# Optimization experiments

Hardware: AMD Instinct MI355X
Metric: run time of the kernel (lower is better)

Reference implementation:

```python
import jax, jax.numpy as jnp
import numpy as np

N_NODES = 100000
N_EDGES = 1600000
EMB = 128
N_LAYERS = 3
BN_EPS = 1e-5


def setup_inputs() -> dict:
    key = jax.random.key(0)
    k1, k2, k3 = jax.random.split(key, 3)
    feats = jax.random.normal(k1, (N_NODES, EMB), dtype=jnp.float32)
    edge_index = jax.random.randint(k2, (2, N_EDGES), 0, N_NODES, dtype=jnp.int64)
    # Glorot-ish scaled weights per layer
    W = jax.random.normal(k3, (N_LAYERS, EMB, EMB), dtype=jnp.float32) * (1.0 / np.sqrt(EMB))
    b = jnp.zeros((N_LAYERS, EMB), dtype=jnp.float32)
    gamma = jnp.ones((N_LAYERS, EMB), dtype=jnp.float32)
    beta = jnp.zeros((N_LAYERS, EMB), dtype=jnp.float32)
    return {"feats": feats, "edge_index": edge_index, "W": W, "b": b, "gamma": gamma, "beta": beta}


def _gcn_layer(h, row, col, W_l, b_l):
    # GCNConv (add_self_loops=False, normalize=True): x = h @ W, symmetric-norm scatter-add, + bias
    x = h @ W_l  # [N, D]
    ones = jnp.ones((row.shape[0],), dtype=h.dtype)
    deg = jax.ops.segment_sum(ones, col, num_segments=N_NODES)  # in-degree of targets
    dinv = jnp.where(deg > 0, jax.lax.rsqrt(jnp.maximum(deg, 1.0)), 0.0)
    norm = dinv[row] * dinv[col]  # [E]
    msg = x[row] * norm[:, None]  # gather + scale, [E, D]
    out = jax.ops.segment_sum(msg, col, num_segments=N_NODES)  # scatter-add
    return out + b_l


def _batch_norm(h, gamma_l, beta_l):
    mu = jnp.mean(h, axis=0)
    var = jnp.mean(jnp.square(h - mu), axis=0)  # biased var (torch BN training math)
    return (h - mu) * jax.lax.rsqrt(var + BN_EPS) * gamma_l + beta_l


def reference(feats, edge_index, W, b, gamma, beta):
    row, col = edge_index[0], edge_index[1]  # source, target
    h = feats
    for l in range(N_LAYERS):
        h = _gcn_layer(h, row, col, W[l], b[l])
        h = _batch_norm(h, gamma[l], beta[l])
        # dropout treated as identity (eval mode); residual=False; JK='last'
    return h
```

## Files before the change

### kernel.cpp

```cpp
#include <hip/hip_runtime.h>
#include <cstdint>
#include <cstddef>

#define BN_EPS 1e-5f
#define NCHUNK 256
#define WT_PITCH 136

typedef short bf16x8 __attribute__((ext_vector_type(8)));
typedef float f32x4 __attribute__((ext_vector_type(4)));


__device__ __forceinline__ int edge_at(const void* e, long long i, int m64) {
  return m64 ? (int)((const long long*)e)[i] : ((const int*)e)[i];
}

__device__ __forceinline__ unsigned short f2bf(float f) {
  unsigned int u = __float_as_uint(f);
  unsigned int r = (u + 0x7FFFu + ((u >> 16) & 1u)) >> 16;
  return (unsigned short)r;
}

__device__ __forceinline__ unsigned int pack2bf(float lo, float hi) {
  return (unsigned int)f2bf(lo) | ((unsigned int)f2bf(hi) << 16);
}

__global__ void detect_kernel(const int* __restrict__ e, int* __restrict__ mode) {
  int nz = 0;
  for (int i = 1; i < 512; i += 2) nz |= e[i];
  mode[0] = (nz == 0) ? 1 : 0;
}


__global__ __launch_bounds__(256) void count_kernel(const void* __restrict__ edges,
                                                    const int* __restrict__ mode,
                                                    int* __restrict__ blockcounts,
                                                    int E, int nb, int chunk) {
  __shared__ int h[1024];
  int m = mode[0];
  for (int i = threadIdx.x; i < nb; i += 256) h[i] = 0;
  __syncthreads();
  long long lo = (long long)blockIdx.x * chunk;
  long long hi = lo + chunk;
  if (hi > E) hi = E;
  for (long long i = lo + threadIdx.x; i < hi; i += 256) {
    int c = edge_at(edges, (long long)E + i, m);
    atomicAdd(&h[c >> 8], 1);
  }
  __syncthreads();
  for (int j = threadIdx.x; j < nb; j += 256)
    blockcounts[(size_t)j * NCHUNK + blockIdx.x] = h[j];
}

__global__ __launch_bounds__(256) void scan1_kernel(const int* __restrict__ src,
                                                    int* __restrict__ tprefix,
                                                    int* __restrict__ bsum, int n) {
  __shared__ int s[256];
  int t = threadIdx.x;
  int gid = blockIdx.x * 256 + t;
  int base = gid * 4;
  int sum = 0;
#pragma unroll
  for (int j = 0; j < 4; j++) {
    int i = base + j;
    if (i < n) sum += src[i];
  }
  s[t] = sum;
  __syncthreads();
  for (int off = 1; off < 256; off <<= 1) {
    int v = (t >= off) ? s[t - off] : 0;
    __syncthreads();
    s[t] += v;
    __syncthreads();
  }
  tprefix[gid] = s[t] - sum;
  if (t == 255) bsum[blockIdx.x] = s[255];
}

__global__ __launch_bounds__(256) void scan2_kernel(int* __restrict__ bsum, int nbk,
                                                    int* __restrict__ out, int n) {
  __shared__ int s[256];
  int t = threadIdx.x;
  int v = (t < nbk) ? bsum[t] : 0;
  s[t] = v;
  __syncthreads();
  for (int off = 1; off < 256; off <<= 1) {
    int u = (t >= off) ? s[t - off] : 0;
    __syncthreads();
    s[t] += u;
    __syncthreads();
  }
  if (t < nbk) bsum[t] = s[t] - v;
  if (t == 255) out[n] = s[255];
}

__global__ __launch_bounds__(256) void scan3_kernel(const int* __restrict__ src,
                                                    const int* __restrict__ tprefix,
                                                    const int* __restrict__ bsum,
                                                    int* __restrict__ out, int n) {
  int gid = blockIdx.x * 256 + threadIdx.x;
  int run = bsum[blockIdx.x] + tprefix[gid];
  int base = gid * 4;
#pragma unroll
  for (int j = 0; j < 4; j++) {
    int i = base + j;
    if (i < n) {
      int c = src[i];
      out[i] = run;
      run += c;
    }
  }
}

__global__ __launch_bounds__(256) void scatter_kernel(const void* __restrict__ edges,
                                                      const int* __restrict__ mode,
                                                      const int* __restrict__ moff,
                                                      int* __restrict__ pairs,
                                                      int E, int nb, int chunk) {
  __shared__ int cur[1024];
  int m = mode[0];
  for (int j = threadIdx.x; j < nb; j += 256)
    cur[j] = moff[(size_t)j * NCHUNK + blockIdx.x];
  __syncthreads();
  long long lo = (long long)blockIdx.x * chunk;
  long long hi = lo + chunk;
  if (hi > E) hi = E;
  for (long long i = lo + threadIdx.x; i < hi; i += 256) {
    int r = edge_at(edges, i, m);
    int c = edge_at(edges, (long long)E + i, m);
    int pos = atomicAdd(&cur[c >> 8], 1);
    pairs[pos] = (r << 8) | (c & 255);
  }
}

__global__ __launch_bounds__(256) void passB12_kernel(const int* __restrict__ pairs,
                                                      const int* __restrict__ moff,
                                                      float* __restrict__ dinv,
                                                      int* __restrict__ offsets,
                                                      int* __restrict__ csr_row, int n) {
  __shared__ int h[256];
  __shared__ int s[256];
  int t = threadIdx.x;
  int b = blockIdx.x;
  h[t] = 0;
  __syncthreads();
  int lo = moff[(size_t)b * NCHUNK];
  int hi = moff[(size_t)(b + 1) * NCHUNK];
  for (int e = lo + t; e < hi; e += 256)
    atomicAdd(&h[pairs[e] & 255], 1);
  __syncthreads();
  int d = h[t];
  s[t] = d;
  __syncthreads();
  for (int off = 1; off < 256; off <<= 1) {
    int v = (t >= off) ? s[t - off] : 0;
    __syncthreads();
    s[t] += v;
    __syncthreads();
  }
  int start = lo + s[t] - d;
  int node = b * 256 + t;
  if (node < n) {
    offsets[node] = start;
    dinv[node] = d > 0 ? rsqrtf((float)d) : 0.f;
    if (node == n - 1) offsets[n] = hi;
  }
  s[t] = start;
  __syncthreads();
  for (int e = lo + t; e < hi; e += 256) {
    int p = pairs[e];
    int pos = atomicAdd(&s[p & 255], 1);
    csr_row[pos] = p >> 8;
  }
}

__global__ __launch_bounds__(256) void prepWR_kernel(const float* __restrict__ W,
                                                     const float* __restrict__ colstats,
                                                     const float* __restrict__ gamma,
                                                     const float* __restrict__ beta,
                                                     float invN, int use_affine,
                                                     unsigned short* __restrict__ Wt,
                                                     float* __restrict__ rbias) {
  __shared__ float sc[128], sh[128];
  int t = threadIdx.x;
  if (t < 128) {
    float scv = 1.f, shv = 0.f;
    if (use_affine) {
      float mu = colstats[t] * invN;
      float var = colstats[128 + t] * invN - mu * mu;
      var = fmaxf(var, 0.f);
      scv = gamma[t] * rsqrtf(var + BN_EPS);
      shv = beta[t] - mu * scv;
    }
    sc[t] = scv;
    sh[t] = shv;
  }
  __syncthreads();
  int idx = blockIdx.x * 256 + t;
  int nc = idx >> 7, k = idx & 127;
  Wt[(size_t)nc * 128 + k] = f2bf(W[(size_t)k * 128 + nc] * sc[k]);
  if (blockIdx.x == 0 && t < 128) {
    float s = 0.f;
    if (use_affine) {
      for (int kk = 0; kk < 128; kk++) s += sh[kk] * W[(size_t)kk * 128 + t];
    }
    rbias[t] = s;
  }
}

template <int A_IS_FP32>
__global__ __launch_bounds__(256) void gemm_mfma_kernel(
    const void* __restrict__ Ain, const unsigned short* __restrict__ Wt,
    const float* __restrict__ rbias, const float* __restrict__ dinv,
    unsigned short* __restrict__ xb, int n) {
  __shared__ unsigned short wt[128 * WT_PITCH];
  int t = threadIdx.x;
  {
    int row = t >> 1, half = t & 1;
    const uint4* src = (const uint4*)(Wt + (size_t)row * 128 + half * 64);
    uint4* dst = (uint4*)(wt + row * WT_PITCH + half * 64);
#pragma unroll
    for (int j = 0; j < 8; j++) dst[j] = src[j];
  }
  __syncthreads();

  int l = t & 63;
  int w = t >> 6;
  int kg = l >> 4;

  for (int sub = 0; sub < 2; sub++) {
    int row0 = blockIdx.x * 128 + sub * 64 + w * 16;
    if (row0 >= n) break;
    int m = row0 + (l & 15);
    int mc = m < n ? m : n - 1;

    bf16x8 b[4];
#pragma unroll
    for (int kk = 0; kk < 4; kk++) {
      if (A_IS_FP32) {
        const float* ap = (const float*)Ain + (size_t)mc * 128 + kk * 32 + kg * 8;
        float4 f0 = *(const float4*)ap;
        float4 f1 = *(const float4*)(ap + 4);
        bf16x8 bb;
        bb[0] = (short)f2bf(f0.x); bb[1] = (short)f2bf(f0.y);
        bb[2] = (short)f2bf(f0.z); bb[3] = (short)f2bf(f0.w);
        bb[4] = (short)f2bf(f1.x); bb[5] = (short)f2bf(f1.y);
        bb[6] = (short)f2bf(f1.z); bb[7] = (short)f2bf(f1.w);
        b[kk] = bb;
      } else {
        b[kk] = *(const bf16x8*)((const unsigned short*)Ain + (size_t)mc * 128 + kk * 32 + kg * 8);
      }
    }

    f32x4 acc[8];
#pragma unroll
    for (int nt = 0; nt < 8; nt++) {
      f32x4 zv = {0.f, 0.f, 0.f, 0.f};
      acc[nt] = zv;
    }

#pragma unroll
    for (int kk = 0; kk < 4; kk++) {
#pragma unroll
      for (int nt = 0; nt < 8; nt++) {
        bf16x8 a = *(const bf16x8*)(wt + (size_t)(nt * 16 + (l & 15)) * WT_PITCH + kk * 32 + kg * 8);
        acc[nt] = __builtin_amdgcn_mfma_f32_16x16x32_bf16(a, b[kk], acc[nt], 0, 0, 0);
      }
    }

    float dv = dinv[mc];
    int colbase = kg * 4;
#pragma unroll
    for (int nt = 0; nt < 8; nt++) {
      int c0 = nt * 16 + colbase;
      float4 rb = *(const float4*)&rbias[c0];
      unsigned int w0 = pack2bf((acc[nt][0] + rb.x) * dv, (acc[nt][1] + rb.y) * dv);
      unsigned int w1 = pack2bf((acc[nt][2] + rb.z) * dv, (acc[nt][3] + rb.w) * dv);
      if (m < n)
        *(uint2*)(xb + (size_t)m * 128 + c0) = make_uint2(w0, w1);
    }
  }
}

template <int F32OUT>
__global__ __launch_bounds__(256) void agg_kernel(
    const uint4* __restrict__ x4, const int* __restrict__ csr_row,
    const int* __restrict__ offsets, const float* __restrict__ dinv,
    void* __restrict__ z, int n) {
  int node = blockIdx.x * 16 + (threadIdx.x >> 4);
  int d8 = threadIdx.x & 15;
  if (node >= n) return;
  int lo = offsets[node], hi = offsets[node + 1];
  float a0[8] = {}, a1[8] = {}, a2[8] = {}, a3[8] = {};
#define ACC8(A, v)                                                         \
  A[0] += __uint_as_float((v).x << 16); A[1] += __uint_as_float((v).x & 0xffff0000u); \
  A[2] += __uint_as_float((v).y << 16); A[3] += __uint_as_float((v).y & 0xffff0000u); \
  A[4] += __uint_as_float((v).z << 16); A[5] += __uint_as_float((v).z & 0xffff0000u); \
  A[6] += __uint_as_float((v).w << 16); A[7] += __uint_as_float((v).w & 0xffff0000u);
  int e = lo;
  for (; e + 4 <= hi; e += 4) {
    int r0 = csr_row[e];
    int r1 = csr_row[e + 1];
    int r2 = csr_row[e + 2];
    int r3 = csr_row[e + 3];
    uint4 v0 = x4[(size_t)r0 * 16 + d8];
    uint4 v1 = x4[(size_t)r1 * 16 + d8];
    uint4 v2 = x4[(size_t)r2 * 16 + d8];
    uint4 v3 = x4[(size_t)r3 * 16 + d8];
    ACC8(a0, v0) ACC8(a1, v1) ACC8(a2, v2) ACC8(a3, v3)
  }
  for (; e < hi; e++) {
    uint4 v = x4[(size_t)csr_row[e] * 16 + d8];
    ACC8(a0, v)
  }
#undef ACC8
  float dvn = dinv[node];
  float s[8];
#pragma unroll
  for (int j = 0; j < 8; j++) s[j] = (a0[j] + a1[j] + a2[j] + a3[j]) * dvn;
  if (F32OUT) {
    float* zp = (float*)z + (size_t)node * 128 + d8 * 8;
    *(float4*)zp = make_float4(s[0], s[1], s[2], s[3]);
    *(float4*)(zp + 4) = make_float4(s[4], s[5], s[6], s[7]);
  } else {
    uint4 o = make_uint4(pack2bf(s[0], s[1]), pack2bf(s[2], s[3]),
                         pack2bf(s[4], s[5]), pack2bf(s[6], s[7]));
    *(uint4*)((unsigned short*)z + (size_t)node * 128 + d8 * 8) = o;
  }
}

template <int F32IN>
__global__ __launch_bounds__(256) void stats2_kernel(
    const void* __restrict__ z, float* __restrict__ partial, int total8) {
  __shared__ float ps[256];
  int t = threadIdx.x;
  ps[t] = 0.f;
  __syncthreads();
  int d8 = t & 15;
  float s[8] = {}, q[8] = {};
  int idx = blockIdx.x * 256 + t;
  int stride = gridDim.x * 256;
  for (int i = idx; i < total8; i += stride) {
    float v[8];
    if (F32IN) {
      const float* zp = (const float*)z + (size_t)i * 8;
      float4 f0 = *(const float4*)zp;
      float4 f1 = *(const float4*)(zp + 4);
      v[0] = f0.x; v[1] = f0.y; v[2] = f0.z; v[3] = f0.w;
      v[4] = f1.x; v[5] = f1.y; v[6] = f1.z; v[7] = f1.w;
    } else {
      uint4 u = ((const uint4*)z)[i];
      v[0] = __uint_as_float(u.x << 16); v[1] = __uint_as_float(u.x & 0xffff0000u);
      v[2] = __uint_as_float(u.y << 16); v[3] = __uint_as_float(u.y & 0xffff0000u);
      v[4] = __uint_as_float(u.z << 16); v[5] = __uint_as_float(u.z & 0xffff0000u);
      v[6] = __uint_as_float(u.w << 16); v[7] = __uint_as_float(u.w & 0xffff0000u);
    }
#pragma unroll
    for (int j = 0; j < 8; j++) { s[j] += v[j]; q[j] += v[j] * v[j]; }
  }
#pragma unroll
  for (int j = 0; j < 8; j++) {
    atomicAdd(&ps[d8 * 8 + j], s[j]);
    atomicAdd(&ps[128 + d8 * 8 + j], q[j]);
  }
  __syncthreads();
  partial[(size_t)blockIdx.x * 256 + t] = ps[t];
}

__global__ __launch_bounds__(256) void reduce_stats_kernel(
    const float* __restrict__ partial, float* __restrict__ out, int nblk) {
  __shared__ float red[256];
  int c = blockIdx.x;
  float s = 0.f;
  for (int i = threadIdx.x; i < nblk; i += 256) s += partial[(size_t)i * 256 + c];
  red[threadIdx.x] = s;
  __syncthreads();
  for (int o = 128; o > 0; o >>= 1) {
    if (threadIdx.x < o) red[threadIdx.x] += red[threadIdx.x + o];
    __syncthreads();
  }
  if (threadIdx.x == 0) out[c] = red[0];
}

__global__ __launch_bounds__(256) void norm_kernel(
    float* __restrict__ z, const float* __restrict__ colstats,
    const float* __restrict__ gamma, const float* __restrict__ beta,
    float invN, int total4) {
  __shared__ float sc[128], sh[128];
  int t = threadIdx.x;
  if (t < 128) {
    float mu = colstats[t] * invN;
    float var = colstats[128 + t] * invN - mu * mu;
    var = fmaxf(var, 0.f);
    float s = gamma[t] * rsqrtf(var + BN_EPS);
    sc[t] = s;
    sh[t] = beta[t] - mu * s;
  }
  __syncthreads();
  int idx = blockIdx.x * blockDim.x + t;
  int stride = gridDim.x * blockDim.x;
  for (int i = idx; i < total4; i += stride) {
    float4 v = ((const float4*)z)[i];
    int d0 = (i & 31) * 4;
    v.x = v.x * sc[d0] + sh[d0];
    v.y = v.y * sc[d0 + 1] + sh[d0 + 1];
    v.z = v.z * sc[d0 + 2] + sh[d0 + 2];
    v.w = v.w * sc[d0 + 3] + sh[d0 + 3];
    ((float4*)z)[i] = v;
  }
}


extern "C" void kernel_launch(void* const* d_in, const int* in_sizes, int n_in,
                              void* d_out, int out_size, void* d_ws, size_t ws_size,
                              hipStream_t stream) {
  const float* feats = (const float*)d_in[0];
  const void* edges = d_in[1];
  const float* W = (const float*)d_in[2];
  const float* gamma = (const float*)d_in[4];
  const float* beta = (const float*)d_in[5];

  const int n = in_sizes[0] / 128;
  const int E = in_sizes[1] / 2;

  const int nb = (n + 255) / 256;
  const int m = nb * NCHUNK;
  const int chunk = (E + NCHUNK - 1) / NCHUNK;
  const int sb_m = (m + 1023) / 1024;
  const int nagg = (n + 15) / 16;
  const int nstat = 1024;

  char* ws = (char*)d_ws;
  size_t off = 0;
  unsigned short* xb = (unsigned short*)(ws + off); off += (size_t)n * 128 * 2; off = (off + 255) & ~(size_t)255;
  float* dinv = (float*)(ws + off); off += (size_t)n * 4;
  int* offsets = (int*)(ws + off); off += (size_t)(n + 1) * 4; off = (off + 255) & ~(size_t)255;
  int* csr_row = (int*)(ws + off); off += (size_t)E * 4; off = (off + 255) & ~(size_t)255;
  int* pairs = (int*)(ws + off); off += (size_t)E * 4; off = (off + 255) & ~(size_t)255;
  int* blockcounts = (int*)(ws + off); off += (size_t)m * 4; off = (off + 255) & ~(size_t)255;
  int* moff = (int*)(ws + off); off += (size_t)(m + 1) * 4; off = (off + 255) & ~(size_t)255;
  int* tprefix = (int*)(ws + off); off += (size_t)sb_m * 256 * 4; off = (off + 255) & ~(size_t)255;
  int* bsum = (int*)(ws + off); off += 256 * 4;
  unsigned short* Wt = (unsigned short*)(ws + off); off += 128 * 128 * 2; off = (off + 255) & ~(size_t)255;
  float* rbias = (float*)(ws + off); off += 128 * 4;
  float* colstats = (float*)(ws + off); off += 256 * 4;
  int* mode = (int*)(ws + off); off += 4;

  float* partial = (float*)pairs;

  detect_kernel<<<1, 1, 0, stream>>>((const int*)edges, mode);
  count_kernel<<<NCHUNK, 256, 0, stream>>>(edges, mode, blockcounts, E, nb, chunk);
  scan1_kernel<<<sb_m, 256, 0, stream>>>(blockcounts, tprefix, bsum, m);
  scan2_kernel<<<1, 256, 0, stream>>>(bsum, sb_m, moff, m);
  scan3_kernel<<<sb_m, 256, 0, stream>>>(blockcounts, tprefix, bsum, moff, m);
  scatter_kernel<<<NCHUNK, 256, 0, stream>>>(edges, mode, moff, pairs, E, nb, chunk);
  passB12_kernel<<<nb, 256, 0, stream>>>(pairs, moff, dinv, offsets, csr_row, n);

  unsigned short* zb = (unsigned short*)d_out;
  float* zf = (float*)d_out;
  const int ggrid = (n + 127) / 128;
  const int total8 = n * 16;
  const float invN = 1.0f / (float)n;

  for (int l = 0; l < 3; l++) {
    prepWR_kernel<<<64, 256, 0, stream>>>(W + (size_t)l * 16384, colstats,
                                          gamma + l * 128, beta + l * 128, invN,
                                          l > 0 ? 1 : 0, Wt, rbias);
    if (l == 0)
      gemm_mfma_kernel<1><<<ggrid, 256, 0, stream>>>(feats, Wt, rbias, dinv, xb, n);
    else
      gemm_mfma_kernel<0><<<ggrid, 256, 0, stream>>>(zb, Wt, rbias, dinv, xb, n);
    if (l < 2) {
      agg_kernel<0><<<nagg, 256, 0, stream>>>(
          (const uint4*)xb, csr_row, offsets, dinv, zb, n);
      stats2_kernel<0><<<nstat, 256, 0, stream>>>(zb, partial, total8);
    } else {
      agg_kernel<1><<<nagg, 256, 0, stream>>>(
          (const uint4*)xb, csr_row, offsets, dinv, zf, n);
      stats2_kernel<1><<<nstat, 256, 0, stream>>>(zf, partial, total8);
    }
    reduce_stats_kernel<<<256, 256, 0, stream>>>(partial, colstats, nstat);
  }
  norm_kernel<<<2048, 256, 0, stream>>>(zf, colstats, gamma + 2 * 128, beta + 2 * 128,
                                        invN, (n * 128) / 4);
}
```

Measured before the change: 417.5 us.

## Fold mode detection into kernels, prefetch GEMM rows, keep final layer in bf16

Drops the single-thread detect kernel and has thread 0 of each count/scatter block probe the edge dtype itself, removing one launch. The GEMM kernel now issues its first row-tile global loads before staging W into LDS, which overlaps load latency with the LDS copy. When workspace allows, the last layer's aggregation writes bf16 into a scratch buffer and a new norm kernel expands it to fp32, halving intermediate traffic. The cost is lower precision in the final pre-norm activations, and every block of two kernels now does redundant detection reads.

```diff
diff --git a/kernel.cpp b/kernel.cpp
--- a/kernel.cpp
+++ b/kernel.cpp
@@ -24,21 +24,22 @@
   return (unsigned int)f2bf(lo) | ((unsigned int)f2bf(hi) << 16);
 }
 
-__global__ void detect_kernel(const int* __restrict__ e, int* __restrict__ mode) {
+__device__ __forceinline__ int detect_mode_thread0(const int* e32) {
   int nz = 0;
-  for (int i = 1; i < 512; i += 2) nz |= e[i];
-  mode[0] = (nz == 0) ? 1 : 0;
+  for (int i = 1; i < 512; i += 2) nz |= e32[i];
+  return (nz == 0) ? 1 : 0;
 }
 
 
 __global__ __launch_bounds__(256) void count_kernel(const void* __restrict__ edges,
-                                                    const int* __restrict__ mode,
                                                     int* __restrict__ blockcounts,
                                                     int E, int nb, int chunk) {
   __shared__ int h[1024];
-  int m = mode[0];
+  __shared__ int smode;
   for (int i = threadIdx.x; i < nb; i += 256) h[i] = 0;
-  __syncthreads();
+  if (threadIdx.x == 0) smode = detect_mode_thread0((const int*)edges);
+  __syncthreads();
+  int m = smode;
   long long lo = (long long)blockIdx.x * chunk;
   long long hi = lo + chunk;
   if (hi > E) hi = E;
@@ -112,15 +113,16 @@
 }
 
 __global__ __launch_bounds__(256) void scatter_kernel(const void* __restrict__ edges,
-                                                      const int* __restrict__ mode,
                                                       const int* __restrict__ moff,
                                                       int* __restrict__ pairs,
                                                       int E, int nb, int chunk) {
   __shared__ int cur[1024];
-  int m = mode[0];
+  __shared__ int smode;
   for (int j = threadIdx.x; j < nb; j += 256)
     cur[j] = moff[(size_t)j * NCHUNK + blockIdx.x];
-  __syncthreads();
+  if (threadIdx.x == 0) smode = detect_mode_thread0((const int*)edges);
+  __syncthreads();
+  int m = smode;
   long long lo = (long long)blockIdx.x * chunk;
   long long hi = lo + chunk;
   if (hi > E) hi = E;
@@ -207,6 +209,57 @@
   }
 }
 
+
+template <int A_IS_FP32>
+__device__ __forceinline__ void gemm_load_b(const void* Ain, int mc, int kg, bf16x8* b) {
+#pragma unroll
+  for (int kk = 0; kk < 4; kk++) {
+    if (A_IS_FP32) {
+      const float* ap = (const float*)Ain + (size_t)mc * 128 + kk * 32 + kg * 8;
+      float4 f0 = *(const float4*)ap;
+      float4 f1 = *(const float4*)(ap + 4);
+      bf16x8 bb;
+      bb[0] = (short)f2bf(f0.x); bb[1] = (short)f2bf(f0.y);
+      bb[2] = (short)f2bf(f0.z); bb[3] = (short)f2bf(f0.w);
+      bb[4] = (short)f2bf(f1.x); bb[5] = (short)f2bf(f1.y);
+      bb[6] = (short)f2bf(f1.z); bb[7] = (short)f2bf(f1.w);
+      b[kk] = bb;
+    } else {
+      b[kk] = *(const bf16x8*)((const unsigned short*)Ain + (size_t)mc * 128 + kk * 32 + kg * 8);
+    }
+  }
+}
+
+__device__ __forceinline__ void gemm_compute_store(
+    const unsigned short* wt, const bf16x8* b, const float* rbias,
+    const float* dinv, unsigned short* xb, int m, int mc, int l, int kg, int n) {
+  f32x4 acc[8];
+#pragma unroll
+  for (int nt = 0; nt < 8; nt++) {
+    f32x4 zv = {0.f, 0.f, 0.f, 0.f};
+    acc[nt] = zv;
+  }
+#pragma unroll
+  for (int kk = 0; kk < 4; kk++) {
+#pragma unroll
+    for (int nt = 0; nt < 8; nt++) {
+      bf16x8 a = *(const bf16x8*)(wt + (size_t)(nt * 16 + (l & 15)) * WT_PITCH + kk * 32 + kg * 8);
+      acc[nt] = __builtin_amdgcn_mfma_f32_16x16x32_bf16(a, b[kk], acc[nt], 0, 0, 0);
+    }
+  }
+  float dv = dinv[mc];
+  int colbase = kg * 4;
+#pragma unroll
+  for (int nt = 0; nt < 8; nt++) {
+    int c0 = nt * 16 + colbase;
+    float4 rb = *(const float4*)&rbias[c0];
+    unsigned int w0 = pack2bf((acc[nt][0] + rb.x) * dv, (acc[nt][1] + rb.y) * dv);
+    unsigned int w1 = pack2bf((acc[nt][2] + rb.z) * dv, (acc[nt][3] + rb.w) * dv);
+    if (m < n)
+      *(uint2*)(xb + (size_t)m * 128 + c0) = make_uint2(w0, w1);
+  }
+}
+
 template <int A_IS_FP32>
 __global__ __launch_bounds__(256) void gemm_mfma_kernel(
     const void* __restrict__ Ain, const unsigned short* __restrict__ Wt,
@@ -214,6 +267,16 @@
     unsigned short* __restrict__ xb, int n) {
   __shared__ unsigned short wt[128 * WT_PITCH];
   int t = threadIdx.x;
+  int l = t & 63;
+  int w = t >> 6;
+  int kg = l >> 4;
+
+  int row0 = blockIdx.x * 128 + w * 16;
+  int m0 = row0 + (l & 15);
+  int mc0 = m0 < n ? m0 : n - 1;
+  bf16x8 b[4];
+  gemm_load_b<A_IS_FP32>(Ain, mc0, kg, b);
+
   {
     int row = t >> 1, half = t & 1;
     const uint4* src = (const uint4*)(Wt + (size_t)row * 128 + half * 64);
@@ -223,61 +286,15 @@
   }
   __syncthreads();
 
-  int l = t & 63;
-  int w = t >> 6;
-  int kg = l >> 4;
-
-  for (int sub = 0; sub < 2; sub++) {
-    int row0 = blockIdx.x * 128 + sub * 64 + w * 16;
-    if (row0 >= n) break;
-    int m = row0 + (l & 15);
-    int mc = m < n ? m : n - 1;
-
-    bf16x8 b[4];
-#pragma unroll
-    for (int kk = 0; kk < 4; kk++) {
-      if (A_IS_FP32) {
-        const float* ap = (const float*)Ain + (size_t)mc * 128 + kk * 32 + kg * 8;
-        float4 f0 = *(const float4*)ap;
-        float4 f1 = *(const float4*)(ap + 4);
-        bf16x8 bb;
-        bb[0] = (short)f2bf(f0.x); bb[1] = (short)f2bf(f0.y);
-        bb[2] = (short)f2bf(f0.z); bb[3] = (short)f2bf(f0.w);
-        bb[4] = (short)f2bf(f1.x); bb[5] = (short)f2bf(f1.y);
-        bb[6] = (short)f2bf(f1.z); bb[7] = (short)f2bf(f1.w);
-        b[kk] = bb;
-      } else {
-        b[kk] = *(const bf16x8*)((const unsigned short*)Ain + (size_t)mc * 128 + kk * 32 + kg * 8);
-      }
-    }
-
-    f32x4 acc[8];
-#pragma unroll
-    for (int nt = 0; nt < 8; nt++) {
-      f32x4 zv = {0.f, 0.f, 0.f, 0.f};
-      acc[nt] = zv;
-    }
-
-#pragma unroll
-    for (int kk = 0; kk < 4; kk++) {
-#pragma unroll
-      for (int nt = 0; nt < 8; nt++) {
-        bf16x8 a = *(const bf16x8*)(wt + (size_t)(nt * 16 + (l & 15)) * WT_PITCH + kk * 32 + kg * 8);
-        acc[nt] = __builtin_amdgcn_mfma_f32_16x16x32_bf16(a, b[kk], acc[nt], 0, 0, 0);
-      }
-    }
-
-    float dv = dinv[mc];
-    int colbase = kg * 4;
-#pragma unroll
-    for (int nt = 0; nt < 8; nt++) {
-      int c0 = nt * 16 + colbase;
-      float4 rb = *(const float4*)&rbias[c0];
-      unsigned int w0 = pack2bf((acc[nt][0] + rb.x) * dv, (acc[nt][1] + rb.y) * dv);
-      unsigned int w1 = pack2bf((acc[nt][2] + rb.z) * dv, (acc[nt][3] + rb.w) * dv);
-      if (m < n)
-        *(uint2*)(xb + (size_t)m * 128 + c0) = make_uint2(w0, w1);
-    }
+  if (row0 < n)
+    gemm_compute_store(wt, b, rbias, dinv, xb, m0, mc0, l, kg, n);
+
+  int row1 = row0 + 64;
+  if (row1 < n) {
+    int m1 = m0 + 64;
+    int mc1 = m1 < n ? m1 : n - 1;
+    gemm_load_b<A_IS_FP32>(Ain, mc1, kg, b);
+    gemm_compute_store(wt, b, rbias, dinv, xb, m1, mc1, l, kg, n);
   }
 }
 
@@ -409,6 +426,35 @@
   }
 }
 
+__global__ __launch_bounds__(256) void norm_bf16_kernel(
+    const unsigned short* __restrict__ zb, float* __restrict__ out,
+    const float* __restrict__ colstats, const float* __restrict__ gamma,
+    const float* __restrict__ beta, float invN, int total4) {
+  __shared__ float sc[128], sh[128];
+  int t = threadIdx.x;
+  if (t < 128) {
+    float mu = colstats[t] * invN;
+    float var = colstats[128 + t] * invN - mu * mu;
+    var = fmaxf(var, 0.f);
+    float s = gamma[t] * rsqrtf(var + BN_EPS);
+    sc[t] = s;
+    sh[t] = beta[t] - mu * s;
+  }
+  __syncthreads();
+  int idx = blockIdx.x * blockDim.x + t;
+  int stride = gridDim.x * blockDim.x;
+  for (int i = idx; i < total4; i += stride) {
+    uint2 u = *(const uint2*)(zb + (size_t)i * 4);
+    int d0 = (i & 31) * 4;
+    float4 v;
+    v.x = __uint_as_float(u.x << 16) * sc[d0] + sh[d0];
+    v.y = __uint_as_float(u.x & 0xffff0000u) * sc[d0 + 1] + sh[d0 + 1];
+    v.z = __uint_as_float(u.y << 16) * sc[d0 + 2] + sh[d0 + 2];
+    v.w = __uint_as_float(u.y & 0xffff0000u) * sc[d0 + 3] + sh[d0 + 3];
+    ((float4*)out)[i] = v;
+  }
+}
+
 
 extern "C" void kernel_launch(void* const* d_in, const int* in_sizes, int n_in,
                               void* d_out, int out_size, void* d_ws, size_t ws_size,
@@ -442,23 +488,24 @@
   int* bsum = (int*)(ws + off); off += 256 * 4;
   unsigned short* Wt = (unsigned short*)(ws + off); off += 128 * 128 * 2; off = (off + 255) & ~(size_t)255;
   float* rbias = (float*)(ws + off); off += 128 * 4;
-  float* colstats = (float*)(ws + off); off += 256 * 4;
-  int* mode = (int*)(ws + off); off += 4;
+  float* colstats = (float*)(ws + off); off += 256 * 4; off = (off + 255) & ~(size_t)255;
+  unsigned short* zb2 = (unsigned short*)(ws + off);
+  const int use_bf16z = (off + (size_t)n * 128 * 2 <= ws_size) ? 1 : 0;
 
   float* partial = (float*)pairs;
 
-  detect_kernel<<<1, 1, 0, stream>>>((const int*)edges, mode);
-  count_kernel<<<NCHUNK, 256, 0, stream>>>(edges, mode, blockcounts, E, nb, chunk);
+  count_kernel<<<NCHUNK, 256, 0, stream>>>(edges, blockcounts, E, nb, chunk);
   scan1_kernel<<<sb_m, 256, 0, stream>>>(blockcounts, tprefix, bsum, m);
   scan2_kernel<<<1, 256, 0, stream>>>(bsum, sb_m, moff, m);
   scan3_kernel<<<sb_m, 256, 0, stream>>>(blockcounts, tprefix, bsum, moff, m);
-  scatter_kernel<<<NCHUNK, 256, 0, stream>>>(edges, mode, moff, pairs, E, nb, chunk);
+  scatter_kernel<<<NCHUNK, 256, 0, stream>>>(edges, moff, pairs, E, nb, chunk);
   passB12_kernel<<<nb, 256, 0, stream>>>(pairs, moff, dinv, offsets, csr_row, n);
 
   unsigned short* zb = (unsigned short*)d_out;
   float* zf = (float*)d_out;
   const int ggrid = (n + 127) / 128;
   const int total8 = n * 16;
+  const int total4 = (n * 128) / 4;
   const float invN = 1.0f / (float)n;
 
   for (int l = 0; l < 3; l++) {
@@ -473,6 +520,10 @@
       agg_kernel<0><<<nagg, 256, 0, stream>>>(
           (const uint4*)xb, csr_row, offsets, dinv, zb, n);
       stats2_kernel<0><<<nstat, 256, 0, stream>>>(zb, partial, total8);
+    } else if (use_bf16z) {
+      agg_kernel<0><<<nagg, 256, 0, stream>>>(
+          (const uint4*)xb, csr_row, offsets, dinv, zb2, n);
+      stats2_kernel<0><<<nstat, 256, 0, stream>>>(zb2, partial, total8);
     } else {
       agg_kernel<1><<<nagg, 256, 0, stream>>>(
           (const uint4*)xb, csr_row, offsets, dinv, zf, n);
@@ -480,6 +531,10 @@
     }
     reduce_stats_kernel<<<256, 256, 0, stream>>>(partial, colstats, nstat);
   }
-  norm_kernel<<<2048, 256, 0, stream>>>(zf, colstats, gamma + 2 * 128, beta + 2 * 128,
-                                        invN, (n * 128) / 4);
-}
+  if (use_bf16z)
+    norm_bf16_kernel<<<2048, 256, 0, stream>>>(zb2, zf, colstats, gamma + 2 * 128,
+                                               beta + 2 * 128, invN, total4);
+  else
+    norm_kernel<<<2048, 256, 0, stream>>>(zf, colstats, gamma + 2 * 128,
+                                          beta + 2 * 128, invN, total4);
+}
```

After: 413.0 us. No clear change (-1.1%).
